# Optimization experiments

Measured on AMD Instinct MI355X. Metric: run time of the kernel, lower is better.

The kernel has to match this reference:

```python
import jax, jax.numpy as jnp
import numpy as np

B, T_V, T_A = 128, 64, 128
E_V, E_A = 1024, 512
H, EMB, C = 1024, 512, 512  # C = input_size - embedding_size
IN = EMB + C               # RNN input size = 1024
VOCAB = 20000


def setup_inputs() -> dict:
    key = jax.random.key(0)
    ks = jax.random.split(key, 26)
    s = 0.02
    inp = {
        "input": jax.random.normal(ks[0], (B, 1, EMB), jnp.float32),
        "enc_visual": jax.random.normal(ks[1], (B, T_V, E_V), jnp.float32),
        "enc_audio": jax.random.normal(ks[2], (B, T_A, E_A), jnp.float32),
        "hidden_state": jax.random.normal(ks[3], (1, B, H), jnp.float32),
        "cell_state": jax.random.normal(ks[4], (1, B, H), jnp.float32),
        # visual attention (Bahdanau): W1:[C,H], W2:[C,E_V], W3:[1,C]
        "W_va1": s * jax.random.normal(ks[5], (C, H), jnp.float32),
        "W_va2": s * jax.random.normal(ks[6], (C, E_V), jnp.float32),
        "W_va3": s * jax.random.normal(ks[7], (1, C), jnp.float32),
        "W_venc": s * jax.random.normal(ks[8], (C, E_V), jnp.float32),
        # audio attention
        "W_aa1": s * jax.random.normal(ks[9], (C, H), jnp.float32),
        "W_aa2": s * jax.random.normal(ks[10], (C, E_A), jnp.float32),
        "W_aa3": s * jax.random.normal(ks[11], (1, C), jnp.float32),
        "W_aenc": s * jax.random.normal(ks[12], (C, E_A), jnp.float32),
        # cross-modal context attention (over 2 context vectors)
        "W_ca1": s * jax.random.normal(ks[13], (C, H), jnp.float32),
        "W_ca2": s * jax.random.normal(ks[14], (C, C), jnp.float32),
        "W_ca3": s * jax.random.normal(ks[15], (1, C), jnp.float32),
        # LSTM-style custom RNN cell params
        "W_ih": s * jax.random.normal(ks[16], (4 * H, IN), jnp.float32),
        "W_hh": s * jax.random.normal(ks[17], (4 * H, H), jnp.float32),
        "b_ih": jnp.zeros((4 * H,), jnp.float32),
        "b_hh": jnp.zeros((4 * H,), jnp.float32),
        # output projection
        "W_out": s * jax.random.normal(ks[18], (VOCAB, H), jnp.float32),
        "b_out": jnp.zeros((VOCAB,), jnp.float32),
    }
    return inp


def _attend(h, enc, W1, W2, W3):
    # h: [B,H]; enc: [B,T,E]. Vectorized Bahdanau attention (original loops over T).
    v1 = h @ W1.T                               # [B,C]
    v2 = jnp.einsum('bte,ce->btc', enc, W2)     # [B,T,C]
    scores = jnp.tanh(v1[:, None, :] + v2) @ W3.T  # [B,T,1]
    attn = jax.nn.softmax(scores[..., 0], axis=1)  # [B,T]
    return jnp.einsum('bt,bte->be', attn, enc)     # [B,E]


def reference(input, enc_visual, enc_audio, hidden_state, cell_state,
              W_va1, W_va2, W_va3, W_venc,
              W_aa1, W_aa2, W_aa3, W_aenc,
              W_ca1, W_ca2, W_ca3,
              W_ih, W_hh, b_ih, b_hh, W_out, b_out):
    h0 = hidden_state[0]   # [B,H]
    c0 = cell_state[0]     # [B,H]

    vc = _attend(h0, enc_visual, W_va1, W_va2, W_va3) @ W_venc.T  # [B,C]
    ac = _attend(h0, enc_audio, W_aa1, W_aa2, W_aa3) @ W_aenc.T   # [B,C]
    all_ctx = jnp.stack([vc, ac], axis=1)                         # [B,2,C]
    final_ctx = _attend(h0, all_ctx, W_ca1, W_ca2, W_ca3)         # [B,C]

    x = jnp.concatenate([input[:, 0, :], jnp.tanh(final_ctx)], axis=-1)  # [B,IN]
    gates = x @ W_ih.T + b_ih + h0 @ W_hh.T + b_hh                 # [B,4H]
    i, f, g, o = jnp.split(gates, 4, axis=-1)
    c_new = jax.nn.sigmoid(f) * c0 + jax.nn.sigmoid(i) * jnp.tanh(g)
    h_new = jax.nn.sigmoid(o) * jnp.tanh(c_new)

    logits = h_new @ W_out.T + b_out                               # [B,V]
    return (logits[:, None, :], h_new[None], c_new[None])
```

## Files before the change

### kernel.cpp

```cpp
#include <hip/hip_runtime.h>
#include <hip/hip_bf16.h>
#include <cstddef>

typedef __attribute__((ext_vector_type(8))) short short8;
typedef __attribute__((ext_vector_type(4))) float f32x4;

static __device__ __forceinline__ short8 pack8(float4 f0, float4 f1) {
    union { __hip_bfloat162 h[4]; short8 s; } u;
    u.h[0] = __float22bfloat162_rn(make_float2(f0.x, f0.y));
    u.h[1] = __float22bfloat162_rn(make_float2(f0.z, f0.w));
    u.h[2] = __float22bfloat162_rn(make_float2(f1.x, f1.y));
    u.h[3] = __float22bfloat162_rn(make_float2(f1.z, f1.w));
    return u.s;
}

static __device__ __forceinline__ void lds_barrier() {
    asm volatile("s_waitcnt lgkmcnt(0)" ::: "memory");
    __builtin_amdgcn_s_barrier();
    asm volatile("" ::: "memory");
}

static __device__ __forceinline__ void sk_body(
    const float* __restrict__ A, int lda,
    const float* __restrict__ W,
    const float* __restrict__ bias, int addbias,
    float* __restrict__ C, int ldc, int N,
    int kbeg, int kend, int n0, int m0)
{
    __shared__ short As[2][128 * 32];
    __shared__ short Ws[2][64 * 32];
    const int tid  = threadIdx.x;
    const int lane = tid & 63;
    const int wave = tid >> 6;
    const int wm = wave * 32;

    f32x4 acc[2][4];
    #pragma unroll
    for (int i = 0; i < 2; ++i)
        #pragma unroll
        for (int j = 0; j < 4; ++j)
            acc[i][j] = (f32x4){0.f, 0.f, 0.f, 0.f};

    const int arow = tid >> 1;
    const int ah   = tid & 1;
    const int afs  = (arow >> 1) & 3;
    const float* gA = A + (size_t)(m0 + arow) * lda + kbeg + ah * 16;
    const int aoff0 = arow * 32 + (((ah * 2)     ^ afs) * 8);
    const int aoff1 = arow * 32 + (((ah * 2 + 1) ^ afs) * 8);

    const int wrow  = tid >> 2;
    const int wslot = tid & 3;
    const int wvalid = (n0 + wrow) < N;
    const float* gW = W + (size_t)(n0 + wrow) * lda + kbeg + wslot * 8;
    const int woff = wrow * 32 + ((wslot ^ ((wrow >> 1) & 3)) * 8);

    const int frow = lane & 15;
    const int hi   = lane >> 4;
    const int fsl  = (hi ^ ((frow >> 1) & 3)) * 8;
    const int ra   = (wm + frow) * 32 + fsl;
    const int rb   = frow * 32 + fsl;

    const int nsteps = (kend - kbeg) >> 5;

    float4 a0_[4], a1_[4], w0_[2], w1_[2];
    #pragma unroll
    for (int q = 0; q < 4; ++q) a0_[q] = *(const float4*)(gA + q * 4);
    #pragma unroll
    for (int q = 0; q < 4; ++q) a1_[q] = *(const float4*)(gA + 32 + q * 4);
    if (wvalid) {
        w0_[0] = *(const float4*)(gW);      w0_[1] = *(const float4*)(gW + 4);
        w1_[0] = *(const float4*)(gW + 32); w1_[1] = *(const float4*)(gW + 36);
    } else {
        w0_[0] = w0_[1] = w1_[0] = w1_[1] = make_float4(0, 0, 0, 0);
    }

    for (int s = 0; s < nsteps; s += 2) {
        {
            short* as = As[0]; short* ws = Ws[0];
            *(short8*)(as + aoff0) = pack8(a0_[0], a0_[1]);
            *(short8*)(as + aoff1) = pack8(a0_[2], a0_[3]);
            *(short8*)(ws + woff)  = pack8(w0_[0], w0_[1]);
            if (s + 2 < nsteps) {
                const float* nA = gA + (s + 2) * 32;
                #pragma unroll
                for (int q = 0; q < 4; ++q) a0_[q] = *(const float4*)(nA + q * 4);
                if (wvalid) {
                    const float* nW = gW + (s + 2) * 32;
                    w0_[0] = *(const float4*)(nW); w0_[1] = *(const float4*)(nW + 4);
                }
            }
            lds_barrier();
            short8 af[2], bf[4];
            #pragma unroll
            for (int i = 0; i < 2; ++i) af[i] = *(const short8*)(as + ra + i * 512);
            #pragma unroll
            for (int j = 0; j < 4; ++j) bf[j] = *(const short8*)(ws + rb + j * 512);
            #pragma unroll
            for (int i = 0; i < 2; ++i)
                #pragma unroll
                for (int j = 0; j < 4; ++j)
                    acc[i][j] = __builtin_amdgcn_mfma_f32_16x16x32_bf16(af[i], bf[j], acc[i][j], 0, 0, 0);
        }
        {
            short* as = As[1]; short* ws = Ws[1];
            *(short8*)(as + aoff0) = pack8(a1_[0], a1_[1]);
            *(short8*)(as + aoff1) = pack8(a1_[2], a1_[3]);
            *(short8*)(ws + woff)  = pack8(w1_[0], w1_[1]);
            if (s + 3 < nsteps) {
                const float* nA = gA + (s + 3) * 32;
                #pragma unroll
                for (int q = 0; q < 4; ++q) a1_[q] = *(const float4*)(nA + q * 4);
                if (wvalid) {
                    const float* nW = gW + (s + 3) * 32;
                    w1_[0] = *(const float4*)(nW); w1_[1] = *(const float4*)(nW + 4);
                }
            }
            lds_barrier();
            short8 af[2], bf[4];
            #pragma unroll
            for (int i = 0; i < 2; ++i) af[i] = *(const short8*)(as + ra + i * 512);
            #pragma unroll
            for (int j = 0; j < 4; ++j) bf[j] = *(const short8*)(ws + rb + j * 512);
            #pragma unroll
            for (int i = 0; i < 2; ++i)
                #pragma unroll
                for (int j = 0; j < 4; ++j)
                    acc[i][j] = __builtin_amdgcn_mfma_f32_16x16x32_bf16(af[i], bf[j], acc[i][j], 0, 0, 0);
        }
    }

    const int cl = lane & 15;
    const int rq = hi * 4;
    #pragma unroll
    for (int j = 0; j < 4; ++j) {
        int gc = n0 + j * 16 + cl;
        if (gc >= N) continue;
        float b = addbias ? bias[gc] : 0.f;
        #pragma unroll
        for (int i = 0; i < 2; ++i) {
            int gr = m0 + wm + i * 16 + rq;
            #pragma unroll
            for (int r = 0; r < 4; ++r)
                atomicAdd(C + (size_t)(gr + r) * ldc + gc, acc[i][j][r] + b);
        }
    }
}

__global__ __launch_bounds__(256) void gemm_sk(
    const float* __restrict__ A, const float* __restrict__ W,
    const float* __restrict__ bias, float* __restrict__ C,
    int N, int K, int kchunk, int ldc)
{
    int kbeg = blockIdx.y * kchunk;
    sk_body(A, K, W, bias, bias != nullptr && blockIdx.y == 0,
            C, ldc, N, kbeg, kbeg + kchunk, blockIdx.x * 64, blockIdx.z * 128);
}

__global__ __launch_bounds__(256) void hproj3_mfma(
    const float* __restrict__ h0,
    const float* __restrict__ Wa, const float* __restrict__ Wb, const float* __restrict__ Wc,
    float* __restrict__ hbase)
{
    int n0g = blockIdx.x * 64;
    int wsel = n0g >> 9;
    const float* W = (wsel == 0) ? Wa : (wsel == 1) ? Wb : Wc;
    float* C = hbase + (size_t)wsel * 128 * 512;
    int kbeg = blockIdx.y * 128;
    sk_body(h0, 1024, W, nullptr, 0, C, 512, 512, kbeg, kbeg + 128, n0g & 511, 0);
}

__global__ __launch_bounds__(256) void ctxproj_mfma(
    const float* __restrict__ attv, const float* __restrict__ Wv,
    const float* __restrict__ atta, const float* __restrict__ Wa,
    float* __restrict__ ctx)
{
    const float* A; const float* W; float* C; int lda, kb, ke;
    if (blockIdx.z == 0) { A = attv; W = Wv; C = ctx;       lda = 1024; kb = blockIdx.y * 128; ke = kb + 128; }
    else                 { A = atta; W = Wa; C = ctx + 512; lda = 512;  kb = blockIdx.y * 64;  ke = kb + 64;  }
    sk_body(A, lda, W, nullptr, 0, C, 1024, 512, kb, ke, blockIdx.x * 64, 0);
}

__global__ __launch_bounds__(256) void gates_mfma(
    const float* __restrict__ xb, const float* __restrict__ W_ih,
    const float* __restrict__ h0, const float* __restrict__ W_hh,
    float* __restrict__ gates)
{
    int pair = blockIdx.y >> 2;
    const float* A = pair ? h0 : xb;
    const float* W = pair ? W_hh : W_ih;
    int kb = (blockIdx.y & 3) * 256;
    sk_body(A, 1024, W, nullptr, 0, gates, 4096, 4096, kb, kb + 256, blockIdx.x * 64, 0);
}

__global__ __launch_bounds__(256) void scores_fused(
    const float* __restrict__ encv, const float* __restrict__ W_va2,
    const float* __restrict__ hv1,  const float* __restrict__ W_va3,
    float* __restrict__ scv,
    const float* __restrict__ enca, const float* __restrict__ W_aa2,
    const float* __restrict__ ha1,  const float* __restrict__ W_aa3,
    float* __restrict__ sca)
{
    __shared__ short As[2][64 * 32];
    __shared__ short Ws[2][128 * 32];

    const float *A, *W, *v1, *W3;
    float* sc;
    int K, tshift, n0, m0;
    int idx = blockIdx.x;
    if (idx < 512) {
        n0 = (idx >> 7) * 128;  m0 = (idx & 127) * 64;
        A = encv; W = W_va2; v1 = hv1; W3 = W_va3; sc = scv;
        K = 1024; tshift = 6;
    } else {
        idx -= 512;
        n0 = (idx >> 8) * 128;  m0 = (idx & 255) * 64;
        A = enca; W = W_aa2; v1 = ha1; W3 = W_aa3; sc = sca;
        K = 512; tshift = 7;
    }

    const int tid  = threadIdx.x;
    const int lane = tid & 63;
    const int wave = tid >> 6;
    const int wm = (wave >> 1) * 32;
    const int wn = (wave & 1) * 64;

    f32x4 acc[2][4];
    #pragma unroll
    for (int i = 0; i < 2; ++i)
        #pragma unroll
        for (int j = 0; j < 4; ++j)
            acc[i][j] = (f32x4){0.f, 0.f, 0.f, 0.f};

    const int arow  = tid >> 2;
    const int aslot = tid & 3;
    const float* gA = A + (size_t)(m0 + arow) * K + aslot * 8;
    const int aoff  = arow * 32 + ((aslot ^ ((arow >> 1) & 3)) * 8);

    const int wrow = tid >> 1;
    const int wh   = tid & 1;
    const int wfs  = (wrow >> 1) & 3;
    const float* gW = W + (size_t)(n0 + wrow) * K + wh * 16;
    const int woff0 = wrow * 32 + (((wh * 2)     ^ wfs) * 8);
    const int woff1 = wrow * 32 + (((wh * 2 + 1) ^ wfs) * 8);

    const int frow = lane & 15;
    const int hi   = lane >> 4;
    const int fsl  = (hi ^ ((frow >> 1) & 3)) * 8;
    const int ra   = (wm + frow) * 32 + fsl;
    const int rb   = (wn + frow) * 32 + fsl;

    const int nsteps = K >> 5;

    float4 a0_[2], a1_[2], w0_[4], w1_[4];
    a0_[0] = *(const float4*)(gA);      a0_[1] = *(const float4*)(gA + 4);
    a1_[0] = *(const float4*)(gA + 32); a1_[1] = *(const float4*)(gA + 36);
    #pragma unroll
    for (int q = 0; q < 4; ++q) w0_[q] = *(const float4*)(gW + q * 4);
    #pragma unroll
    for (int q = 0; q < 4; ++q) w1_[q] = *(const float4*)(gW + 32 + q * 4);

    for (int s = 0; s < nsteps; s += 2) {
        {
            short* as = As[0]; short* ws = Ws[0];
            *(short8*)(as + aoff)  = pack8(a0_[0], a0_[1]);
            *(short8*)(ws + woff0) = pack8(w0_[0], w0_[1]);
            *(short8*)(ws + woff1) = pack8(w0_[2], w0_[3]);
            if (s + 2 < nsteps) {
                const float* nA = gA + (s + 2) * 32;
                a0_[0] = *(const float4*)(nA); a0_[1] = *(const float4*)(nA + 4);
                const float* nW = gW + (s + 2) * 32;
                #pragma unroll
                for (int q = 0; q < 4; ++q) w0_[q] = *(const float4*)(nW + q * 4);
            }
            lds_barrier();
            short8 af[2], bf[4];
            #pragma unroll
            for (int i = 0; i < 2; ++i) af[i] = *(const short8*)(as + ra + i * 512);
            #pragma unroll
            for (int j = 0; j < 4; ++j) bf[j] = *(const short8*)(ws + rb + j * 512);
            #pragma unroll
            for (int i = 0; i < 2; ++i)
                #pragma unroll
                for (int j = 0; j < 4; ++j)
                    acc[i][j] = __builtin_amdgcn_mfma_f32_16x16x32_bf16(af[i], bf[j], acc[i][j], 0, 0, 0);
        }
        {
            short* as = As[1]; short* ws = Ws[1];
            *(short8*)(as + aoff)  = pack8(a1_[0], a1_[1]);
            *(short8*)(ws + woff0) = pack8(w1_[0], w1_[1]);
            *(short8*)(ws + woff1) = pack8(w1_[2], w1_[3]);
            if (s + 3 < nsteps) {
                const float* nA = gA + (s + 3) * 32;
                a1_[0] = *(const float4*)(nA); a1_[1] = *(const float4*)(nA + 4);
                const float* nW = gW + (s + 3) * 32;
                #pragma unroll
                for (int q = 0; q < 4; ++q) w1_[q] = *(const float4*)(nW + q * 4);
            }
            lds_barrier();
            short8 af[2], bf[4];
            #pragma unroll
            for (int i = 0; i < 2; ++i) af[i] = *(const short8*)(as + ra + i * 512);
            #pragma unroll
            for (int j = 0; j < 4; ++j) bf[j] = *(const short8*)(ws + rb + j * 512);
            #pragma unroll
            for (int i = 0; i < 2; ++i)
                #pragma unroll
                for (int j = 0; j < 4; ++j)
                    acc[i][j] = __builtin_amdgcn_mfma_f32_16x16x32_bf16(af[i], bf[j], acc[i][j], 0, 0, 0);
        }
    }

    const int cl = lane & 15;
    const int rq = hi * 4;
    #pragma unroll
    for (int i = 0; i < 2; ++i) {
        #pragma unroll
        for (int r = 0; r < 4; ++r) {
            int gr = m0 + wm + i * 16 + rq + r;
            const float* v1row = v1 + (size_t)(gr >> tshift) * 512;
            float p = 0.f;
            #pragma unroll
            for (int j = 0; j < 4; ++j) {
                int gc = n0 + wn + j * 16 + cl;
                p += tanhf(v1row[gc] + acc[i][j][r]) * W3[gc];
            }
            p += __shfl_xor(p, 1, 64);
            p += __shfl_xor(p, 2, 64);
            p += __shfl_xor(p, 4, 64);
            p += __shfl_xor(p, 8, 64);
            if (cl == 0) atomicAdd(sc + gr, p);
        }
    }
}

__global__ __launch_bounds__(256) void attend_out2(
    const float* __restrict__ scv, const float* __restrict__ encv, float* __restrict__ attv,
    const float* __restrict__ sca, const float* __restrict__ enca, float* __restrict__ atta)
{
    const float* sc; const float* enc; float* out;
    int T, E, ec;
    if (blockIdx.y < 4) { sc = scv; enc = encv; out = attv; T = 64;  E = 1024; ec = blockIdx.y; }
    else                { sc = sca; enc = enca; out = atta; T = 128; E = 512;  ec = blockIdx.y - 4; }

    __shared__ float ew[128];
    const int b = blockIdx.x, tid = threadIdx.x;
    __shared__ float raw[128];
    if (tid < T) raw[tid] = sc[(size_t)b * T + tid];
    __syncthreads();
    float m = -1e30f;
    for (int t = 0; t < T; ++t) m = fmaxf(m, raw[t]);
    if (tid < T) ew[tid] = __expf(raw[tid] - m);
    __syncthreads();
    float sum = 0.f;
    for (int t = 0; t < T; ++t) sum += ew[t];
    const float inv = 1.f / sum;

    const int e = ec * 256 + tid;
    const float* encb = enc + (size_t)b * T * E + e;
    float acc = 0.f;
    for (int t = 0; t < T; ++t)
        acc += ew[t] * encb[(size_t)t * E];
    out[(size_t)b * E + e] = acc * inv;
}

__global__ __launch_bounds__(256) void cross_kernel(
    const float* __restrict__ hc1, const float* __restrict__ v2c,
    const float* __restrict__ W3, const float* __restrict__ ctx,
    const float* __restrict__ inp, float* __restrict__ x)
{
    const int C = 512;
    __shared__ float red[256];
    __shared__ float aw[2];
    const int b = blockIdx.x, tid = threadIdx.x;

    float p0 = 0.f, p1 = 0.f;
    for (int c = tid; c < C; c += 256) {
        float h = hc1[(size_t)b * C + c], w = W3[c];
        p0 += tanhf(h + v2c[(size_t)(b * 2 + 0) * C + c]) * w;
        p1 += tanhf(h + v2c[(size_t)(b * 2 + 1) * C + c]) * w;
    }
    red[tid] = p0; __syncthreads();
    for (int s = 128; s; s >>= 1) { if (tid < s) red[tid] += red[tid + s]; __syncthreads(); }
    float s0 = red[0];
    __syncthreads();
    red[tid] = p1; __syncthreads();
    for (int s = 128; s; s >>= 1) { if (tid < s) red[tid] += red[tid + s]; __syncthreads(); }
    if (tid == 0) {
        float s1 = red[0];
        float m = fmaxf(s0, s1);
        float e0 = __expf(s0 - m), e1 = __expf(s1 - m);
        float inv = 1.f / (e0 + e1);
        aw[0] = e0 * inv; aw[1] = e1 * inv;
    }
    __syncthreads();
    float a0 = aw[0], a1 = aw[1];
    for (int c = tid; c < C; c += 256) {
        float fc = a0 * ctx[(size_t)(b * 2 + 0) * C + c]
                 + a1 * ctx[(size_t)(b * 2 + 1) * C + c];
        x[(size_t)b * 1024 + 512 + c] = tanhf(fc);
        x[(size_t)b * 1024 + c] = inp[(size_t)b * 512 + c];
    }
}

__global__ __launch_bounds__(256) void lstm_kernel(
    const float* __restrict__ gates, const float* __restrict__ c0,
    const float* __restrict__ b_ih, const float* __restrict__ b_hh,
    float* __restrict__ hout, float* __restrict__ cout)
{
    const int idx = blockIdx.x * 256 + threadIdx.x;
    const int b = idx >> 10, h = idx & 1023;
    const float* g = gates + (size_t)b * 4096;
    float gi = g[h]        + b_ih[h]        + b_hh[h];
    float gf = g[1024 + h] + b_ih[1024 + h] + b_hh[1024 + h];
    float gg = g[2048 + h] + b_ih[2048 + h] + b_hh[2048 + h];
    float go = g[3072 + h] + b_ih[3072 + h] + b_hh[3072 + h];
    float si = 1.f / (1.f + __expf(-gi));
    float sf = 1.f / (1.f + __expf(-gf));
    float so = 1.f / (1.f + __expf(-go));
    float cn = sf * c0[idx] + si * tanhf(gg);
    float hn = so * tanhf(cn);
    cout[idx] = cn;
    hout[idx] = hn;
}

extern "C" void kernel_launch(void* const* d_in, const int* in_sizes, int n_in,
                              void* d_out, int out_size, void* d_ws, size_t ws_size,
                              hipStream_t stream)
{
    const float* inp    = (const float*)d_in[0];
    const float* encv   = (const float*)d_in[1];
    const float* enca   = (const float*)d_in[2];
    const float* h0     = (const float*)d_in[3];
    const float* c0     = (const float*)d_in[4];
    const float* W_va1  = (const float*)d_in[5];
    const float* W_va2  = (const float*)d_in[6];
    const float* W_va3  = (const float*)d_in[7];
    const float* W_venc = (const float*)d_in[8];
    const float* W_aa1  = (const float*)d_in[9];
    const float* W_aa2  = (const float*)d_in[10];
    const float* W_aa3  = (const float*)d_in[11];
    const float* W_aenc = (const float*)d_in[12];
    const float* W_ca1  = (const float*)d_in[13];
    const float* W_ca2  = (const float*)d_in[14];
    const float* W_ca3  = (const float*)d_in[15];
    const float* W_ih   = (const float*)d_in[16];
    const float* W_hh   = (const float*)d_in[17];
    const float* b_ih   = (const float*)d_in[18];
    const float* b_hh   = (const float*)d_in[19];
    const float* W_out  = (const float*)d_in[20];
    const float* b_out  = (const float*)d_in[21];
    float* out = (float*)d_out;

    float* ws = (float*)d_ws;
    float* hv1  = ws;  ws += 128 * 512;
    float* ha1  = ws;  ws += 128 * 512;
    float* hc1  = ws;  ws += 128 * 512;
    float* scv  = ws;  ws += 128 * 64;
    float* sca  = ws;  ws += 128 * 128;
    float* ctx  = ws;  ws += 128 * 2 * 512;
    float* v2c  = ws;  ws += 128 * 2 * 512;
    float* gates= ws;  ws += (size_t)128 * 4096;
    size_t zero_floats = (size_t)(ws - (float*)d_ws);
    float* xb   = ws;  ws += 128 * 1024;
    float* attv = ws;  ws += 128 * 1024;
    float* atta = ws;  ws += 128 * 512;

    dim3 blk(256);

    hipMemsetAsync(d_ws, 0, zero_floats * sizeof(float), stream);
    hipMemsetAsync(out, 0, (size_t)128 * 20000 * sizeof(float), stream);

    hproj3_mfma<<<dim3(24, 8), blk, 0, stream>>>(h0, W_va1, W_aa1, W_ca1, hv1);
    scores_fused<<<dim3(1536), blk, 0, stream>>>(encv, W_va2, hv1, W_va3, scv,
                                                 enca, W_aa2, ha1, W_aa3, sca);
    attend_out2<<<dim3(128, 6), blk, 0, stream>>>(scv, encv, attv, sca, enca, atta);
    ctxproj_mfma<<<dim3(8, 8, 2), blk, 0, stream>>>(attv, W_venc, atta, W_aenc, ctx);
    gemm_sk<<<dim3(8, 4, 2), blk, 0, stream>>>(ctx, W_ca2, nullptr, v2c, 512, 512, 128, 512);
    cross_kernel<<<128, blk, 0, stream>>>(hc1, v2c, W_ca3, ctx, inp, xb);
    gates_mfma<<<dim3(64, 8), blk, 0, stream>>>(xb, W_ih, h0, W_hh, gates);
    float* hout = out + 2560000;
    float* cout = out + 2560000 + 131072;
    lstm_kernel<<<512, blk, 0, stream>>>(gates, c0, b_ih, b_hh, hout, cout);
    gemm_sk<<<dim3(313, 2, 1), blk, 0, stream>>>(hout, W_out, b_out, out, 20000, 1024, 512, 20000);
}
```

Before: 380.8 us.

## Pre-convert encoder/attention weights to bf16 and use direct global-to-LDS loads in scores GEMM

Adds a conversion kernel that turns enc_visual, enc_audio, W_va2 and W_aa2 into bf16 copies in workspace. The scores GEMM then streams these through global_load_lds straight into double-buffered LDS and uses larger 128x128 tiles with a 4x4 MFMA accumulator per wave, halving the block count. The aim is to remove the per-step register fp32 loads, packing and LDS stores from the scores kernel and to improve data reuse. In exchange it adds an extra pass that reads all the fp32 encoder data and writes a bf16 copy each call. The sk_body changes only swap float4 for an equivalent vector type.

```diff
diff --git a/kernel.cpp b/kernel.cpp
--- a/kernel.cpp
+++ b/kernel.cpp
@@ -5,7 +5,11 @@
 typedef __attribute__((ext_vector_type(8))) short short8;
 typedef __attribute__((ext_vector_type(4))) float f32x4;
 
-static __device__ __forceinline__ short8 pack8(float4 f0, float4 f1) {
+static __device__ __forceinline__ f32x4 ldg(const float* p) {
+    return *(const f32x4*)p;
+}
+
+static __device__ __forceinline__ short8 pack8(f32x4 f0, f32x4 f1) {
     union { __hip_bfloat162 h[4]; short8 s; } u;
     u.h[0] = __float22bfloat162_rn(make_float2(f0.x, f0.y));
     u.h[1] = __float22bfloat162_rn(make_float2(f0.z, f0.w));
@@ -14,6 +18,12 @@
     return u.s;
 }
 
+static __device__ __forceinline__ void gload16(const short* g, short* l) {
+    __builtin_amdgcn_global_load_lds(
+        (const __attribute__((address_space(1))) void*)g,
+        (__attribute__((address_space(3))) void*)l, 16, 0, 0);
+}
+
 static __device__ __forceinline__ void lds_barrier() {
     asm volatile("s_waitcnt lgkmcnt(0)" ::: "memory");
     __builtin_amdgcn_s_barrier();
@@ -62,16 +72,16 @@
 
     const int nsteps = (kend - kbeg) >> 5;
 
-    float4 a0_[4], a1_[4], w0_[2], w1_[2];
-    #pragma unroll
-    for (int q = 0; q < 4; ++q) a0_[q] = *(const float4*)(gA + q * 4);
-    #pragma unroll
-    for (int q = 0; q < 4; ++q) a1_[q] = *(const float4*)(gA + 32 + q * 4);
+    f32x4 a0_[4], a1_[4], w0_[2], w1_[2];
+    #pragma unroll
+    for (int q = 0; q < 4; ++q) a0_[q] = ldg(gA + q * 4);
+    #pragma unroll
+    for (int q = 0; q < 4; ++q) a1_[q] = ldg(gA + 32 + q * 4);
     if (wvalid) {
-        w0_[0] = *(const float4*)(gW);      w0_[1] = *(const float4*)(gW + 4);
-        w1_[0] = *(const float4*)(gW + 32); w1_[1] = *(const float4*)(gW + 36);
+        w0_[0] = ldg(gW);      w0_[1] = ldg(gW + 4);
+        w1_[0] = ldg(gW + 32); w1_[1] = ldg(gW + 36);
     } else {
-        w0_[0] = w0_[1] = w1_[0] = w1_[1] = make_float4(0, 0, 0, 0);
+        w0_[0] = w0_[1] = w1_[0] = w1_[1] = (f32x4){0.f, 0.f, 0.f, 0.f};
     }
 
     for (int s = 0; s < nsteps; s += 2) {
@@ -83,10 +93,10 @@
             if (s + 2 < nsteps) {
                 const float* nA = gA + (s + 2) * 32;
                 #pragma unroll
-                for (int q = 0; q < 4; ++q) a0_[q] = *(const float4*)(nA + q * 4);
+                for (int q = 0; q < 4; ++q) a0_[q] = ldg(nA + q * 4);
                 if (wvalid) {
                     const float* nW = gW + (s + 2) * 32;
-                    w0_[0] = *(const float4*)(nW); w0_[1] = *(const float4*)(nW + 4);
+                    w0_[0] = ldg(nW); w0_[1] = ldg(nW + 4);
                 }
             }
             lds_barrier();
@@ -109,10 +119,10 @@
             if (s + 3 < nsteps) {
                 const float* nA = gA + (s + 3) * 32;
                 #pragma unroll
-                for (int q = 0; q < 4; ++q) a1_[q] = *(const float4*)(nA + q * 4);
+                for (int q = 0; q < 4; ++q) a1_[q] = ldg(nA + q * 4);
                 if (wvalid) {
                     const float* nW = gW + (s + 3) * 32;
-                    w1_[0] = *(const float4*)(nW); w1_[1] = *(const float4*)(nW + 4);
+                    w1_[0] = ldg(nW); w1_[1] = ldg(nW + 4);
                 }
             }
             lds_barrier();
@@ -192,136 +202,124 @@
     sk_body(A, 1024, W, nullptr, 0, gates, 4096, 4096, kb, kb + 256, blockIdx.x * 64, 0);
 }
 
+__global__ __launch_bounds__(256) void cvt_bf16(
+    const float* __restrict__ encv, const float* __restrict__ enca,
+    const float* __restrict__ wv2,  const float* __restrict__ wa2,
+    short* __restrict__ oev, short* __restrict__ oea,
+    short* __restrict__ owv, short* __restrict__ owa)
+{
+    int bid = blockIdx.x;
+    const float* src; short* dst; int lb;
+    if (bid < 4096)      { src = encv; dst = oev; lb = bid; }
+    else if (bid < 8192) { src = enca; dst = oea; lb = bid - 4096; }
+    else if (bid < 8448) { src = wv2;  dst = owv; lb = bid - 8192; }
+    else                 { src = wa2;  dst = owa; lb = bid - 8448; }
+    size_t off = ((size_t)lb * 256 + threadIdx.x) * 8;
+    f32x4 f0 = *(const f32x4*)(src + off);
+    f32x4 f1 = *(const f32x4*)(src + off + 4);
+    *(short8*)(dst + off) = pack8(f0, f1);
+}
+
 __global__ __launch_bounds__(256) void scores_fused(
-    const float* __restrict__ encv, const float* __restrict__ W_va2,
+    const short* __restrict__ Av, const short* __restrict__ Wv,
     const float* __restrict__ hv1,  const float* __restrict__ W_va3,
     float* __restrict__ scv,
-    const float* __restrict__ enca, const float* __restrict__ W_aa2,
+    const short* __restrict__ Aa, const short* __restrict__ Wa,
     const float* __restrict__ ha1,  const float* __restrict__ W_aa3,
     float* __restrict__ sca)
 {
-    __shared__ short As[2][64 * 32];
-    __shared__ short Ws[2][128 * 32];
-
-    const float *A, *W, *v1, *W3;
+    __shared__ short As[2][4096];
+    __shared__ short Ws[2][4096];
+
+    const short *A, *W; const float *v1, *W3;
     float* sc;
     int K, tshift, n0, m0;
     int idx = blockIdx.x;
-    if (idx < 512) {
-        n0 = (idx >> 7) * 128;  m0 = (idx & 127) * 64;
-        A = encv; W = W_va2; v1 = hv1; W3 = W_va3; sc = scv;
+    if (idx < 256) {
+        n0 = (idx >> 6) * 128;  m0 = (idx & 63) * 128;
+        A = Av; W = Wv; v1 = hv1; W3 = W_va3; sc = scv;
         K = 1024; tshift = 6;
     } else {
-        idx -= 512;
-        n0 = (idx >> 8) * 128;  m0 = (idx & 255) * 64;
-        A = enca; W = W_aa2; v1 = ha1; W3 = W_aa3; sc = sca;
+        idx -= 256;
+        n0 = (idx >> 7) * 128;  m0 = (idx & 127) * 128;
+        A = Aa; W = Wa; v1 = ha1; W3 = W_aa3; sc = sca;
         K = 512; tshift = 7;
     }
 
     const int tid  = threadIdx.x;
     const int lane = tid & 63;
     const int wave = tid >> 6;
-    const int wm = (wave >> 1) * 32;
-    const int wn = (wave & 1) * 64;
-
-    f32x4 acc[2][4];
-    #pragma unroll
-    for (int i = 0; i < 2; ++i)
+    const int wr = wave >> 1;
+    const int wc = wave & 1;
+
+    f32x4 acc[4][4];
+    #pragma unroll
+    for (int i = 0; i < 4; ++i)
         #pragma unroll
         for (int j = 0; j < 4; ++j)
             acc[i][j] = (f32x4){0.f, 0.f, 0.f, 0.f};
 
-    const int arow  = tid >> 2;
-    const int aslot = tid & 3;
-    const float* gA = A + (size_t)(m0 + arow) * K + aslot * 8;
-    const int aoff  = arow * 32 + ((aslot ^ ((arow >> 1) & 3)) * 8);
-
-    const int wrow = tid >> 1;
-    const int wh   = tid & 1;
-    const int wfs  = (wrow >> 1) & 3;
-    const float* gW = W + (size_t)(n0 + wrow) * K + wh * 16;
-    const int woff0 = wrow * 32 + (((wh * 2)     ^ wfs) * 8);
-    const int woff1 = wrow * 32 + (((wh * 2 + 1) ^ wfs) * 8);
+    const int srow = lane >> 2;
+    const int slsw = (lane & 3) ^ ((lane >> 3) & 3);
+    const short* gA0 = A + (size_t)(m0 + wave * 16 + srow) * K + slsw * 8;
+    const short* gA1 = gA0 + (size_t)64 * K;
+    const short* gW0 = W + (size_t)(n0 + wave * 16 + srow) * K + slsw * 8;
+    const short* gW1 = gW0 + (size_t)64 * K;
+    const int ldsw = wave * 512;
 
     const int frow = lane & 15;
     const int hi   = lane >> 4;
     const int fsl  = (hi ^ ((frow >> 1) & 3)) * 8;
-    const int ra   = (wm + frow) * 32 + fsl;
-    const int rb   = (wn + frow) * 32 + fsl;
+    const int raBase = (wr * 64 + frow) * 32 + fsl;
+    const int rbBase = (wc * 64 + frow) * 32 + fsl;
 
     const int nsteps = K >> 5;
 
-    float4 a0_[2], a1_[2], w0_[4], w1_[4];
-    a0_[0] = *(const float4*)(gA);      a0_[1] = *(const float4*)(gA + 4);
-    a1_[0] = *(const float4*)(gA + 32); a1_[1] = *(const float4*)(gA + 36);
-    #pragma unroll
-    for (int q = 0; q < 4; ++q) w0_[q] = *(const float4*)(gW + q * 4);
-    #pragma unroll
-    for (int q = 0; q < 4; ++q) w1_[q] = *(const float4*)(gW + 32 + q * 4);
-
-    for (int s = 0; s < nsteps; s += 2) {
-        {
-            short* as = As[0]; short* ws = Ws[0];
-            *(short8*)(as + aoff)  = pack8(a0_[0], a0_[1]);
-            *(short8*)(ws + woff0) = pack8(w0_[0], w0_[1]);
-            *(short8*)(ws + woff1) = pack8(w0_[2], w0_[3]);
-            if (s + 2 < nsteps) {
-                const float* nA = gA + (s + 2) * 32;
-                a0_[0] = *(const float4*)(nA); a0_[1] = *(const float4*)(nA + 4);
-                const float* nW = gW + (s + 2) * 32;
-                #pragma unroll
-                for (int q = 0; q < 4; ++q) w0_[q] = *(const float4*)(nW + q * 4);
-            }
-            lds_barrier();
-            short8 af[2], bf[4];
-            #pragma unroll
-            for (int i = 0; i < 2; ++i) af[i] = *(const short8*)(as + ra + i * 512);
-            #pragma unroll
-            for (int j = 0; j < 4; ++j) bf[j] = *(const short8*)(ws + rb + j * 512);
-            #pragma unroll
-            for (int i = 0; i < 2; ++i)
-                #pragma unroll
-                for (int j = 0; j < 4; ++j)
-                    acc[i][j] = __builtin_amdgcn_mfma_f32_16x16x32_bf16(af[i], bf[j], acc[i][j], 0, 0, 0);
-        }
-        {
-            short* as = As[1]; short* ws = Ws[1];
-            *(short8*)(as + aoff)  = pack8(a1_[0], a1_[1]);
-            *(short8*)(ws + woff0) = pack8(w1_[0], w1_[1]);
-            *(short8*)(ws + woff1) = pack8(w1_[2], w1_[3]);
-            if (s + 3 < nsteps) {
-                const float* nA = gA + (s + 3) * 32;
-                a1_[0] = *(const float4*)(nA); a1_[1] = *(const float4*)(nA + 4);
-                const float* nW = gW + (s + 3) * 32;
-                #pragma unroll
-                for (int q = 0; q < 4; ++q) w1_[q] = *(const float4*)(nW + q * 4);
-            }
-            lds_barrier();
-            short8 af[2], bf[4];
-            #pragma unroll
-            for (int i = 0; i < 2; ++i) af[i] = *(const short8*)(as + ra + i * 512);
-            #pragma unroll
-            for (int j = 0; j < 4; ++j) bf[j] = *(const short8*)(ws + rb + j * 512);
-            #pragma unroll
-            for (int i = 0; i < 2; ++i)
-                #pragma unroll
-                for (int j = 0; j < 4; ++j)
-                    acc[i][j] = __builtin_amdgcn_mfma_f32_16x16x32_bf16(af[i], bf[j], acc[i][j], 0, 0, 0);
-        }
+    gload16(gA0, As[0] + ldsw);
+    gload16(gA1, As[0] + 2048 + ldsw);
+    gload16(gW0, Ws[0] + ldsw);
+    gload16(gW1, Ws[0] + 2048 + ldsw);
+
+    int cur = 0;
+    for (int s = 0; s < nsteps; ++s) {
+        int nk = (s + 1 < nsteps ? s + 1 : s) * 32;
+        gload16(gA0 + nk, As[cur ^ 1] + ldsw);
+        gload16(gA1 + nk, As[cur ^ 1] + 2048 + ldsw);
+        gload16(gW0 + nk, Ws[cur ^ 1] + ldsw);
+        gload16(gW1 + nk, Ws[cur ^ 1] + 2048 + ldsw);
+        asm volatile("s_waitcnt vmcnt(4)" ::: "memory");
+        __builtin_amdgcn_s_barrier();
+        __builtin_amdgcn_sched_barrier(0);
+
+        const short* as = As[cur];
+        const short* ws = Ws[cur];
+        short8 af[4], bf[4];
+        #pragma unroll
+        for (int i = 0; i < 4; ++i) af[i] = *(const short8*)(as + raBase + i * 512);
+        #pragma unroll
+        for (int j = 0; j < 4; ++j) bf[j] = *(const short8*)(ws + rbBase + j * 512);
+        #pragma unroll
+        for (int i = 0; i < 4; ++i)
+            #pragma unroll
+            for (int j = 0; j < 4; ++j)
+                acc[i][j] = __builtin_amdgcn_mfma_f32_16x16x32_bf16(af[i], bf[j], acc[i][j], 0, 0, 0);
+        __builtin_amdgcn_sched_barrier(0);
+        __builtin_amdgcn_s_barrier();
+        cur ^= 1;
     }
 
     const int cl = lane & 15;
     const int rq = hi * 4;
     #pragma unroll
-    for (int i = 0; i < 2; ++i) {
+    for (int i = 0; i < 4; ++i) {
         #pragma unroll
         for (int r = 0; r < 4; ++r) {
-            int gr = m0 + wm + i * 16 + rq + r;
+            int gr = m0 + wr * 64 + i * 16 + rq + r;
             const float* v1row = v1 + (size_t)(gr >> tshift) * 512;
             float p = 0.f;
             #pragma unroll
             for (int j = 0; j < 4; ++j) {
-                int gc = n0 + wn + j * 16 + cl;
+                int gc = n0 + wc * 64 + j * 16 + cl;
                 p += tanhf(v1row[gc] + acc[i][j][r]) * W3[gc];
             }
             p += __shfl_xor(p, 1, 64);
@@ -464,15 +462,21 @@
     float* xb   = ws;  ws += 128 * 1024;
     float* attv = ws;  ws += 128 * 1024;
     float* atta = ws;  ws += 128 * 512;
+    short* encv_bf = (short*)ws;  ws += 8388608 / 2;
+    short* enca_bf = (short*)ws;  ws += 8388608 / 2;
+    short* wv2_bf  = (short*)ws;  ws += 524288 / 2;
+    short* wa2_bf  = (short*)ws;  ws += 262144 / 2;
 
     dim3 blk(256);
 
     hipMemsetAsync(d_ws, 0, zero_floats * sizeof(float), stream);
     hipMemsetAsync(out, 0, (size_t)128 * 20000 * sizeof(float), stream);
 
+    cvt_bf16<<<dim3(8576), blk, 0, stream>>>(encv, enca, W_va2, W_aa2,
+                                             encv_bf, enca_bf, wv2_bf, wa2_bf);
     hproj3_mfma<<<dim3(24, 8), blk, 0, stream>>>(h0, W_va1, W_aa1, W_ca1, hv1);
-    scores_fused<<<dim3(1536), blk, 0, stream>>>(encv, W_va2, hv1, W_va3, scv,
-                                                 enca, W_aa2, ha1, W_aa3, sca);
+    scores_fused<<<dim3(768), blk, 0, stream>>>(encv_bf, wv2_bf, hv1, W_va3, scv,
+                                                enca_bf, wa2_bf, ha1, W_aa3, sca);
     attend_out2<<<dim3(128, 6), blk, 0, stream>>>(scv, encv, attv, sca, enca, atta);
     ctxproj_mfma<<<dim3(8, 8, 2), blk, 0, stream>>>(attv, W_venc, atta, W_aenc, ctx);
     gemm_sk<<<dim3(8, 4, 2), blk, 0, stream>>>(ctx, W_ca2, nullptr, v2c, 512, 512, 128, 512);
```

Measured after the change: 374.6 us. Within noise of the previous version (-1.6%).
